# Optimization experiments

Measured on AMD Instinct MI355X. Metric: run time of the kernel, lower is better.

The kernel has to match this reference:

```python
import jax, jax.numpy as jnp
import numpy as np

NUM_HEADS = 12
LN_EPS = 1e-5
SM_EPS = 1e-6


def layer_norm(x, w, b):
    m = x.mean(-1, keepdims=True)
    v = ((x - m) ** 2).mean(-1, keepdims=True)
    return (x - m) / jnp.sqrt(v + LN_EPS) * w + b


def softmax_with_policy(attn, policy):
    # attn: [B,H,N,N], policy: [B,N,1]
    B, H, N, _ = attn.shape
    attn_policy = policy.reshape(B, 1, 1, N)
    eye = jnp.eye(N, dtype=attn.dtype)[None, None]
    attn_policy = attn_policy + (1.0 - attn_policy) * eye
    m = attn.max(axis=-1, keepdims=True)
    e = jnp.exp(attn - m) * attn_policy
    return (e + SM_EPS / N) / (e.sum(axis=-1, keepdims=True) + SM_EPS)


def create_ys(ncdf, n_ref):
    # ncdf: [B, N-1]; returns ys: [B, n_ref-1]
    B = ncdf.shape[0]
    ys = jnp.linspace(0.0, 1.0, n_ref - 1, dtype=ncdf.dtype)[None, :]
    ys_start = jnp.min(ncdf + (ncdf == 0).astype(ncdf.dtype) * 1e8, axis=1, keepdims=True)
    steps = jnp.arange(n_ref - 1, dtype=ncdf.dtype)[None, :]
    return ys_start + (ys * (n_ref - 2) - ys_start * steps) / (n_ref - 2)


def get_unique_indices(indices, max_value):
    # duplicate indices are replaced by max_value, then re-sorted
    B = indices.shape[0]
    s = jnp.sort(indices, axis=1)
    shifted = jnp.concatenate([s[:, 1:], jnp.ones((B, 1), s.dtype)], axis=1)
    uniq = jnp.where(shifted == s, max_value, s)
    return jnp.sort(uniq, axis=1)


def ats_block(x, policy, norm1_w, norm1_b, qkv_w, proj_w, proj_b,
              norm2_w, norm2_b, fc1_w, fc1_b, fc2_w, fc2_b,
              n_tokens, n_ref_tokens):
    B, N, C = x.shape
    H = NUM_HEADS
    dh = C // H
    scale = dh ** -0.5

    xn = layer_norm(x, norm1_w, norm1_b)
    qkv = (xn @ qkv_w).reshape(B, N, 3, H, dh).transpose(2, 0, 3, 1, 4)  # [3,B,H,N,dh]
    qkv = qkv * policy[None, :, None, :, :]
    q, k, v = qkv[0], qkv[1], qkv[2]

    attn = softmax_with_policy(jnp.einsum('bhnd,bhmd->bhnm', q, k) * scale, policy)

    # --- score assignment ---
    v_norm = jnp.linalg.norm(v.transpose(0, 2, 1, 3).reshape(B, N, C), axis=2)  # [B,N]
    sig = attn[:, :, 0, :].sum(axis=1) * v_norm      # CLS attention row summed over heads
    sig = sig[:, 1:]
    sig = sig / sig.sum(axis=1, keepdims=True)
    order = jnp.argsort(sig, axis=1)                 # ascending
    sorted_scores = jnp.take_along_axis(sig, order, axis=1)

    # --- inverse transform sampling ---
    cdf = jnp.cumsum(sorted_scores, axis=1)
    cmin = cdf.min(axis=1, keepdims=True)
    cmax = cdf.max(axis=1, keepdims=True)
    ncdf = (cdf - cmin) / (cmax - cmin)              # [B, N-1]
    ys = create_ys(ncdf, n_ref_tokens)               # [B, n_ref-1]
    diff = (n_ref_tokens - 1) - (N - 1)
    ncdf_p = jnp.pad(ncdf, ((0, 0), (diff, 0))) if diff > 0 else ncdf
    tokens_to_pick = jnp.argmin(jnp.abs(ys[:, :, None] - ncdf_p[:, None, :]), axis=2) - diff

    uniq = get_unique_indices(tokens_to_pick, N - 1)[:, :N - 1]
    ui = uniq[:, :n_tokens - 1]                      # [B, n_tokens-1]

    # reorder attn rows / raw tokens by significance order, pad a zero row at N-1
    oidx = jnp.broadcast_to(order[:, None, :, None], (B, H, N - 1, N))
    attn_sorted = jnp.take_along_axis(attn[:, :, 1:, :], oidx, axis=2)
    attn_tmp = jnp.pad(attn_sorted, ((0, 0), (0, 0), (0, 1), (0, 0)))
    rx_sorted = jnp.take_along_axis(x[:, 1:, :], jnp.broadcast_to(order[:, :, None], (B, N - 1, C)), axis=1)
    rx_tmp = jnp.pad(rx_sorted, ((0, 0), (0, 1), (0, 0)))

    uidx = jnp.broadcast_to(ui[:, None, :, None], (B, H, n_tokens - 1, N))
    attn_sel = jnp.take_along_axis(attn_tmp, uidx, axis=2)
    rx_sel = jnp.take_along_axis(rx_tmp, jnp.broadcast_to(ui[:, :, None], (B, n_tokens - 1, C)), axis=1)

    attn_new = jnp.concatenate([attn[:, :, 0:1, :], attn_sel], axis=2)     # [B,H,n_tokens,N]
    selected_x = jnp.concatenate([x[:, 0:1, :], rx_sel], axis=1)           # [B,n_tokens,C]
    pol_new = (ui != N - 1).astype(x.dtype)[:, :, None]
    pol_new = jnp.pad(pol_new, ((0, 0), (1, 0), (0, 0)), constant_values=1.0)  # [B,n_tokens,1]

    out = jnp.einsum('bhnm,bhmd->bhnd', attn_new, v)
    out = out.transpose(0, 2, 1, 3).reshape(B, n_tokens, C)
    out = (out @ proj_w + proj_b) * pol_new

    x2 = selected_x + out
    h = jax.nn.gelu(layer_norm(x2, norm2_w, norm2_b) @ fc1_w + fc1_b, approximate=False)
    x2 = x2 + (h @ fc2_w + fc2_b) * pol_new
    return x2, pol_new


def setup_inputs() -> dict:
    key = jax.random.key(0)
    ks = jax.random.split(key, 6)
    B, N, C = 8, 785, 768
    init = lambda k, sh, fan: jax.random.normal(k, sh, jnp.float32) * (fan ** -0.5)
    return {
        'x': jax.random.normal(ks[0], (B, N, C), jnp.float32),
        'policy': jnp.ones((B, N, 1), jnp.float32),
        'norm1_w': jnp.ones((C,), jnp.float32),
        'norm1_b': jnp.zeros((C,), jnp.float32),
        'qkv_w': init(ks[1], (C, 3 * C), C),
        'proj_w': init(ks[2], (C, C), C),
        'proj_b': jnp.zeros((C,), jnp.float32),
        'norm2_w': jnp.ones((C,), jnp.float32),
        'norm2_b': jnp.zeros((C,), jnp.float32),
        'fc1_w': init(ks[3], (C, 4 * C), C),
        'fc1_b': jnp.zeros((4 * C,), jnp.float32),
        'fc2_w': init(ks[4], (4 * C, C), 4 * C),
        'fc2_b': jnp.zeros((C,), jnp.float32),
        'n_tokens': 393,
        'n_ref_tokens': 785,
    }


def reference(x, policy, norm1_w, norm1_b, qkv_w, proj_w, proj_b,
              norm2_w, norm2_b, fc1_w, fc1_b, fc2_w, fc2_b,
              n_tokens, n_ref_tokens):
    return ats_block(x, policy, norm1_w, norm1_b, qkv_w, proj_w, proj_b,
                     norm2_w, norm2_b, fc1_w, fc1_b, fc2_w, fc2_b,
                     int(n_tokens), int(n_ref_tokens))
```

## Files before the change

kernel.cpp:

```cpp
#include <hip/hip_runtime.h>
#include <hip/hip_bf16.h>
#include <float.h>
#include <math.h>
#include <stdint.h>

constexpr int B_   = 8;
constexpr int N_   = 785;
constexpr int C_   = 768;
constexpr int H_   = 12;
constexpr int DH_  = 64;
constexpr int NT_  = 393;
constexpr int QKVC = 3 * C_;
constexpr int BN   = B_ * N_;
constexpr int BT   = B_ * NT_;
constexpr int MSEL = N_ - 1;
constexpr float  SCALE_F = 0.125f;
constexpr double LNEPS   = 1e-5;
constexpr double SMEPS   = 1e-6;

#define DEV static __device__ __forceinline__

typedef __hip_bfloat16 bf16;
typedef __attribute__((ext_vector_type(8))) short frag8;
typedef __attribute__((ext_vector_type(4))) float facc4;

DEV double blockReduceSumD(double v, double* scratch, int nw) {
#pragma unroll
  for (int o = 32; o; o >>= 1) v += __shfl_xor(v, o);
  int lane = threadIdx.x & 63, wid = threadIdx.x >> 6;
  __syncthreads();
  if (lane == 0) scratch[wid] = v;
  __syncthreads();
  double r = scratch[0];
  for (int i = 1; i < nw; i++) r += scratch[i];
  return r;
}
DEV double blockReduceMaxD(double v, double* scratch, int nw) {
#pragma unroll
  for (int o = 32; o; o >>= 1) v = fmax(v, __shfl_xor(v, o));
  int lane = threadIdx.x & 63, wid = threadIdx.x >> 6;
  __syncthreads();
  if (lane == 0) scratch[wid] = v;
  __syncthreads();
  double r = scratch[0];
  for (int i = 1; i < nw; i++) r = fmax(r, scratch[i]);
  return r;
}
DEV float blockReduceSumF(float v, float* scratch, int nw) {
#pragma unroll
  for (int o = 32; o; o >>= 1) v += __shfl_xor(v, o);
  int lane = threadIdx.x & 63, wid = threadIdx.x >> 6;
  __syncthreads();
  if (lane == 0) scratch[wid] = v;
  __syncthreads();
  float r = scratch[0];
  for (int i = 1; i < nw; i++) r += scratch[i];
  return r;
}
DEV float blockReduceMaxF(float v, float* scratch, int nw) {
#pragma unroll
  for (int o = 32; o; o >>= 1) v = fmaxf(v, __shfl_xor(v, o));
  int lane = threadIdx.x & 63, wid = threadIdx.x >> 6;
  __syncthreads();
  if (lane == 0) scratch[wid] = v;
  __syncthreads();
  float r = scratch[0];
  for (int i = 1; i < nw; i++) r = fmaxf(r, scratch[i]);
  return r;
}

__global__ __launch_bounds__(256) void ln1_kernel(
    const float* __restrict__ x, const float* __restrict__ w, const float* __restrict__ b,
    double* __restrict__ xn64, bf16* __restrict__ xnb) {
  int row = blockIdx.x;
  int t = threadIdx.x;
  __shared__ double scr[8];
  const float* xr = x + (size_t)row * C_;
  double vals[3];
#pragma unroll
  for (int i = 0; i < 3; i++) vals[i] = (double)xr[t + i * 256];
  double s = vals[0] + vals[1] + vals[2];
  s = blockReduceSumD(s, scr, 4);
  double mean = s / (double)C_;
  double vs = 0.0;
#pragma unroll
  for (int i = 0; i < 3; i++) { double d = vals[i] - mean; vs += d * d; }
  vs = blockReduceSumD(vs, scr, 4);
  double inv = 1.0 / sqrt(vs / (double)C_ + LNEPS);
#pragma unroll
  for (int i = 0; i < 3; i++) {
    int c = t + i * 256;
    double o = (vals[i] - mean) * inv * (double)w[c] + (double)b[c];
    xn64[(size_t)row * C_ + c] = o;
    xnb[(size_t)row * C_ + c] = __float2bfloat16((float)o);
  }
}

__global__ __launch_bounds__(256) void transpose_bf16(
    const float* __restrict__ W, bf16* __restrict__ Wt, int K, int N) {
  __shared__ float tile[32][33];
  int k0 = blockIdx.y * 32, n0 = blockIdx.x * 32;
  int tx = threadIdx.x & 31, ty = threadIdx.x >> 5;
  for (int i = ty; i < 32; i += 8) {
    int k = k0 + i, n = n0 + tx;
    tile[i][tx] = (k < K && n < N) ? W[(size_t)k * N + n] : 0.f;
  }
  __syncthreads();
  for (int i = ty; i < 32; i += 8) {
    int n = n0 + i, k = k0 + tx;
    if (n < N && k < K) Wt[(size_t)n * K + k] = __float2bfloat16(tile[tx][i]);
  }
}

__global__ __launch_bounds__(256) void gemm_bf16(
    const bf16* __restrict__ A, const bf16* __restrict__ Bt,
    float* __restrict__ Cc, const float* __restrict__ bias,
    const float* __restrict__ rowscale, int M, int K, int Ncols) {
  __shared__ short As[64][40];
  __shared__ short Bs[64][40];
  const short* Ap = (const short*)A;
  const short* Bp = (const short*)Bt;
  int t = threadIdx.x;
  int n0 = blockIdx.x * 64;
  int m0 = blockIdx.y * 64;
  int w = t >> 6, l = t & 63;
  int srow = t >> 2;
  int koff = (t & 3) * 8;
  facc4 acc[4] = {{0, 0, 0, 0}, {0, 0, 0, 0}, {0, 0, 0, 0}, {0, 0, 0, 0}};
  int frow = (l & 15);
  int fk = (l >> 4) * 8;
  for (int k0 = 0; k0 < K; k0 += 32) {
    {
      int4 av = make_int4(0, 0, 0, 0);
      if (m0 + srow < M)
        av = *(const int4*)(Ap + (size_t)(m0 + srow) * K + k0 + koff);
      *(int4*)(&As[srow][koff]) = av;
      int4 bv = *(const int4*)(Bp + (size_t)(n0 + srow) * K + k0 + koff);
      *(int4*)(&Bs[srow][koff]) = bv;
    }
    __syncthreads();
    frag8 a = *(frag8*)(&As[w * 16 + frow][fk]);
#pragma unroll
    for (int nt = 0; nt < 4; nt++) {
      frag8 bfr = *(frag8*)(&Bs[nt * 16 + frow][fk]);
      acc[nt] = __builtin_amdgcn_mfma_f32_16x16x32_bf16(a, bfr, acc[nt], 0, 0, 0);
    }
    __syncthreads();
  }
#pragma unroll
  for (int nt = 0; nt < 4; nt++) {
#pragma unroll
    for (int reg = 0; reg < 4; reg++) {
      int row = m0 + w * 16 + (l >> 4) * 4 + reg;
      int col = n0 + nt * 16 + (l & 15);
      if (row < M) {
        float v = acc[nt][reg];
        if (bias) v += bias[col];
        if (rowscale) v *= rowscale[row];
        Cc[(size_t)row * Ncols + col] = v;
      }
    }
  }
}

__global__ __launch_bounds__(256) void q0_kernel(
    const double* __restrict__ xn64, const float* __restrict__ qkvw,
    const float* __restrict__ policy, double* __restrict__ q064) {
  int b = blockIdx.x;
  int jc = blockIdx.y;
  int t = threadIdx.x;
  int jl = t & 63, ks = t >> 6;
  __shared__ double x0[C_];
  __shared__ double part[4][64];
  for (int i = t; i < C_; i += 256) x0[i] = xn64[(size_t)(b * N_) * C_ + i];
  __syncthreads();
  int j = jc * 64 + jl;
  const float* wp = qkvw + j;
  double a = 0.0;
  int c0 = ks * 192;
#pragma unroll 8
  for (int c = c0; c < c0 + 192; c++) a += x0[c] * (double)wp[(size_t)c * QKVC];
  part[ks][jl] = a;
  __syncthreads();
  if (t < 64) {
    double pol = (double)policy[b * N_];
    q064[b * C_ + jc * 64 + t] =
        (part[0][t] + part[1][t] + part[2][t] + part[3][t]) * pol;
  }
}

__global__ __launch_bounds__(256) void g_kernel(
    const double* __restrict__ q064, const float* __restrict__ qkvw,
    double* __restrict__ g64) {
  int bh = blockIdx.x;
  int b = bh / H_, h = bh % H_;
  int t = threadIdx.x;
  __shared__ double qh[DH_];
  if (t < DH_) qh[t] = q064[b * C_ + h * DH_ + t];
  __syncthreads();
  for (int c = t; c < C_; c += 256) {
    const float* wp = qkvw + (size_t)c * QKVC + C_ + h * DH_;
    double a = 0.0;
#pragma unroll 8
    for (int d = 0; d < DH_; d++) a += qh[d] * (double)wp[d];
    g64[(size_t)bh * C_ + c] = a;
  }
}

__global__ __launch_bounds__(256) void logits_kernel(
    const double* __restrict__ xn64, const double* __restrict__ g64,
    const float* __restrict__ policy, double* __restrict__ l64) {
  int row = blockIdx.x;
  int b = row / N_;
  int n = row % N_;
  int t = threadIdx.x;
  int w = t >> 6, lane = t & 63;
  __shared__ double xr[C_];
  for (int i = t; i < C_; i += 256) xr[i] = xn64[(size_t)row * C_ + i];
  __syncthreads();
  double pol = (double)policy[row];
#pragma unroll
  for (int hh = 0; hh < 3; hh++) {
    int h = w + hh * 4;
    const double* gp = g64 + (size_t)(b * H_ + h) * C_;
    double p = 0.0;
#pragma unroll 4
    for (int i = lane; i < C_; i += 64) p += xr[i] * gp[i];
#pragma unroll
    for (int o = 32; o; o >>= 1) p += __shfl_xor(p, o);
    if (lane == 0) l64[(size_t)(b * H_ + h) * N_ + n] = 0.125 * pol * p;
  }
}

__global__ __launch_bounds__(256) void vnorm_kernel(
    const double* __restrict__ xn64, const float* __restrict__ qkvw,
    const float* __restrict__ policy, double* __restrict__ vnorm2) {
  __shared__ double scr[8];
  int r0 = blockIdx.x * 8;
  int t = threadIdx.x;
  double acc[8][3] = {};
  const double* xb = xn64 + (size_t)r0 * C_;
  for (int c = 0; c < C_; c += 2) {
    const float* wp0 = qkvw + (size_t)c * QKVC + 2 * C_;
    const float* wp1 = wp0 + QKVC;
    double w00 = (double)wp0[t], w01 = (double)wp0[t + 256], w02 = (double)wp0[t + 512];
    double w10 = (double)wp1[t], w11 = (double)wp1[t + 256], w12 = (double)wp1[t + 512];
#pragma unroll
    for (int r = 0; r < 8; r++) {
      double x0 = xb[(size_t)r * C_ + c];
      double x1 = xb[(size_t)r * C_ + c + 1];
      acc[r][0] += x0 * w00; acc[r][1] += x0 * w01; acc[r][2] += x0 * w02;
      acc[r][0] += x1 * w10; acc[r][1] += x1 * w11; acc[r][2] += x1 * w12;
    }
  }
#pragma unroll
  for (int r = 0; r < 8; r++) {
    double p = acc[r][0] * acc[r][0] + acc[r][1] * acc[r][1] + acc[r][2] * acc[r][2];
    double s = blockReduceSumD(p, scr, 4);
    if (t == 0) {
      double pol = (double)policy[r0 + r];
      vnorm2[r0 + r] = s * pol * pol;
    }
  }
}

__global__ __launch_bounds__(256) void softmax0_kernel(
    double* __restrict__ l64, const float* __restrict__ policy) {
  int bh = blockIdx.x;
  int b = bh / H_;
  double* lp = l64 + (size_t)bh * N_;
  __shared__ double scr[8];
  int t = threadIdx.x;
  double mx = -1e300;
  for (int n = t; n < N_; n += 256) mx = fmax(mx, lp[n]);
  mx = blockReduceMaxD(mx, scr, 4);
  double ssum = 0.0;
  for (int n = t; n < N_; n += 256) {
    double pol = (double)policy[b * N_ + n];
    double w = (n == 0) ? 1.0 : pol;
    double e = exp(lp[n] - mx) * w;
    lp[n] = e;
    ssum += e;
  }
  ssum = blockReduceSumD(ssum, scr, 4);
  double denom = ssum + SMEPS;
  double addc = SMEPS / (double)N_;
  for (int n = t; n < N_; n += 256) lp[n] = (lp[n] + addc) / denom;
}

__global__ __launch_bounds__(1024) void select_kernel(
    const double* __restrict__ p0, const double* __restrict__ vnorm2,
    int* __restrict__ selidx, float* __restrict__ poln, float* __restrict__ out_pol) {
  int b = blockIdx.x;
  int t = threadIdx.x;
  __shared__ double sigv[MSEL];
  __shared__ double svals[MSEL];
  __shared__ double nc[MSEL];
  __shared__ int    ord[MSEL];
  __shared__ int    pick[MSEL];
  __shared__ int    spick[MSEL];
  __shared__ int    uq[MSEL];
  __shared__ int    suq[MSEL];
  __shared__ double sh_ys;

  if (t < MSEL) {
    int n = t + 1;
    double s = 0.0;
#pragma unroll
    for (int h = 0; h < H_; h++) s += p0[(size_t)(b * H_ + h) * N_ + n];
    sigv[t] = s * sqrt(vnorm2[b * N_ + n]);
  }
  __syncthreads();
  if (t < MSEL) {
    double v = sigv[t];
    int rank = 0;
    for (int i = 0; i < MSEL; i++) {
      double vi = sigv[i];
      rank += (vi < v) || (vi == v && i < t);
    }
    ord[rank] = t;
    svals[rank] = v;
  }
  __syncthreads();
  if (t == 0) {
    double a = 0.0;
    for (int i = 0; i < MSEL; i++) { a += svals[i]; svals[i] = a; }
  }
  __syncthreads();
  {
    double c0 = svals[0], cN = svals[MSEL - 1];
    if (t < MSEL) nc[t] = (svals[t] - c0) / (cN - c0);
  }
  __syncthreads();
  if (t == 0) {
    double m = 1e300;
    for (int i = 0; i < MSEL; i++) {
      double v = nc[i];
      if (v == 0.0) v += 100000000.0;
      m = fmin(m, v);
    }
    sh_ys = m;
  }
  __syncthreads();
  if (t < MSEL) {
    double s = sh_ys;
    double ysj = (t == MSEL - 1) ? 1.0 : (double)t / 783.0;
    double y = s + (ysj * 783.0 - s * (double)t) / 783.0;
    double bd = 1e300;
    int bi = 0;
    for (int i = 0; i < MSEL; i++) {
      double d = fabs(y - nc[i]);
      if (d < bd) { bd = d; bi = i; }
    }
    pick[t] = bi;
  }
  __syncthreads();
  if (t < MSEL) {
    int p = pick[t];
    int rank = 0;
    for (int i = 0; i < MSEL; i++) {
      int pi = pick[i];
      rank += (pi < p) || (pi == p && i < t);
    }
    spick[rank] = p;
  }
  __syncthreads();
  if (t < MSEL) {
    int s = spick[t];
    int nxt = (t < MSEL - 1) ? spick[t + 1] : 1;
    uq[t] = (nxt == s) ? MSEL : s;
  }
  __syncthreads();
  if (t < MSEL) {
    int u = uq[t];
    int rank = 0;
    for (int i = 0; i < MSEL; i++) {
      int ui = uq[i];
      rank += (ui < u) || (ui == u && i < t);
    }
    suq[rank] = u;
  }
  __syncthreads();
  if (t < NT_) {
    int sel, polI;
    if (t == 0) { sel = 0; polI = 1; }
    else {
      int ut = suq[t - 1];
      polI = (ut != MSEL) ? 1 : 0;
      sel = polI ? (ord[ut] + 1) : -1;
    }
    selidx[b * NT_ + t] = sel;
    poln[b * NT_ + t] = (float)polI;
    out_pol[b * NT_ + t] = (float)polI;
  }
}

__global__ __launch_bounds__(256) void flash_kernel(
    const float* __restrict__ qkv, const int* __restrict__ selidx,
    const float* __restrict__ policy, bf16* __restrict__ attn_bf) {
  int bh = blockIdx.y;
  int b = bh / H_, h = bh % H_;
  int j0 = blockIdx.x * 64;
  int t = threadIdx.x;
  __shared__ float Qs[64][68];
  __shared__ float KVs[64][68];
  __shared__ float Ps[64][68];
  __shared__ float Vsum[64];
  int lm = t >> 2;
  int kb = (t & 3) * 16;
  {
    int j = j0 + lm;
    int r = (j < NT_) ? selidx[b * NT_ + j] : -1;
    if (r < 0) r = 0;
    const float* qp = qkv + (size_t)(b * N_ + r) * QKVC + h * DH_ + kb;
    float4 v0 = *(const float4*)(qp + 0);
    float4 v1 = *(const float4*)(qp + 4);
    float4 v2 = *(const float4*)(qp + 8);
    float4 v3 = *(const float4*)(qp + 12);
    Qs[kb + 0][lm] = v0.x; Qs[kb + 1][lm] = v0.y; Qs[kb + 2][lm] = v0.z; Qs[kb + 3][lm] = v0.w;
    Qs[kb + 4][lm] = v1.x; Qs[kb + 5][lm] = v1.y; Qs[kb + 6][lm] = v1.z; Qs[kb + 7][lm] = v1.w;
    Qs[kb + 8][lm] = v2.x; Qs[kb + 9][lm] = v2.y; Qs[kb +10][lm] = v2.z; Qs[kb +11][lm] = v2.w;
    Qs[kb +12][lm] = v3.x; Qs[kb +13][lm] = v3.y; Qs[kb +14][lm] = v3.z; Qs[kb +15][lm] = v3.w;
  }
  if (t < 64) Vsum[t] = 0.f;
  int tm = (t >> 4) << 2, tn = (t & 15) << 2;
  int rrow[4];
#pragma unroll
  for (int i = 0; i < 4; i++) {
    int j = j0 + tm + i;
    rrow[i] = (j < NT_) ? selidx[b * NT_ + j] : -1;
  }
  float m_run[4] = {-1e30f, -1e30f, -1e30f, -1e30f};
  float s_run[4] = {0.f, 0.f, 0.f, 0.f};
  float O[4][4] = {{0.f}};
  for (int n0 = 0; n0 < 832; n0 += 64) {
    __syncthreads();
    {
      int n = n0 + lm;
      bool ok = n < N_;
      const float* kp = qkv + (size_t)(b * N_ + (ok ? n : 0)) * QKVC + C_ + h * DH_ + kb;
      float4 v0 = ok ? *(const float4*)(kp + 0)  : make_float4(0, 0, 0, 0);
      float4 v1 = ok ? *(const float4*)(kp + 4)  : make_float4(0, 0, 0, 0);
      float4 v2 = ok ? *(const float4*)(kp + 8)  : make_float4(0, 0, 0, 0);
      float4 v3 = ok ? *(const float4*)(kp + 12) : make_float4(0, 0, 0, 0);
      KVs[kb + 0][lm] = v0.x; KVs[kb + 1][lm] = v0.y; KVs[kb + 2][lm] = v0.z; KVs[kb + 3][lm] = v0.w;
      KVs[kb + 4][lm] = v1.x; KVs[kb + 5][lm] = v1.y; KVs[kb + 6][lm] = v1.z; KVs[kb + 7][lm] = v1.w;
      KVs[kb + 8][lm] = v2.x; KVs[kb + 9][lm] = v2.y; KVs[kb +10][lm] = v2.z; KVs[kb +11][lm] = v2.w;
      KVs[kb +12][lm] = v3.x; KVs[kb +13][lm] = v3.y; KVs[kb +14][lm] = v3.z; KVs[kb +15][lm] = v3.w;
    }
    __syncthreads();
    float S[4][4] = {{0.f}};
#pragma unroll 16
    for (int k = 0; k < 64; k++) {
      float a0 = Qs[k][tm + 0], a1 = Qs[k][tm + 1], a2 = Qs[k][tm + 2], a3 = Qs[k][tm + 3];
      float b0 = KVs[k][tn + 0], b1 = KVs[k][tn + 1], b2 = KVs[k][tn + 2], b3 = KVs[k][tn + 3];
      S[0][0] += a0 * b0; S[0][1] += a0 * b1; S[0][2] += a0 * b2; S[0][3] += a0 * b3;
      S[1][0] += a1 * b0; S[1][1] += a1 * b1; S[1][2] += a1 * b2; S[1][3] += a1 * b3;
      S[2][0] += a2 * b0; S[2][1] += a2 * b1; S[2][2] += a2 * b2; S[2][3] += a2 * b3;
      S[3][0] += a3 * b0; S[3][1] += a3 * b1; S[3][2] += a3 * b2; S[3][3] += a3 * b3;
    }
    float tmax[4];
#pragma unroll
    for (int i = 0; i < 4; i++) {
      float mx = -1e30f;
#pragma unroll
      for (int jj = 0; jj < 4; jj++) {
        int n = n0 + tn + jj;
        float v = (n < N_) ? S[i][jj] * SCALE_F : -1e30f;
        S[i][jj] = v;
        mx = fmaxf(mx, v);
      }
      tmax[i] = mx;
    }
#pragma unroll
    for (int o = 1; o < 16; o <<= 1) {
#pragma unroll
      for (int i = 0; i < 4; i++) tmax[i] = fmaxf(tmax[i], __shfl_xor(tmax[i], o));
    }
    float m_new[4], scl[4], psum[4];
#pragma unroll
    for (int i = 0; i < 4; i++) {
      m_new[i] = fmaxf(m_run[i], tmax[i]);
      scl[i] = expf(m_run[i] - m_new[i]);
      psum[i] = 0.f;
    }
    float polv[4];
#pragma unroll
    for (int jj = 0; jj < 4; jj++) {
      int n = n0 + tn + jj;
      polv[jj] = (n < N_) ? policy[b * N_ + n] : 0.f;
    }
#pragma unroll
    for (int i = 0; i < 4; i++) {
#pragma unroll
      for (int jj = 0; jj < 4; jj++) {
        int n = n0 + tn + jj;
        float w = (n == rrow[i]) ? 1.f : polv[jj];
        float e = expf(S[i][jj] - m_new[i]) * w;
        S[i][jj] = e;
        psum[i] += e;
      }
    }
#pragma unroll
    for (int o = 1; o < 16; o <<= 1) {
#pragma unroll
      for (int i = 0; i < 4; i++) psum[i] += __shfl_xor(psum[i], o);
    }
#pragma unroll
    for (int i = 0; i < 4; i++) {
      s_run[i] = s_run[i] * scl[i] + psum[i];
      m_run[i] = m_new[i];
    }
    __syncthreads();
#pragma unroll
    for (int i = 0; i < 4; i++) {
#pragma unroll
      for (int jj = 0; jj < 4; jj++) Ps[tn + jj][tm + i] = S[i][jj];
    }
    {
      int n = n0 + lm;
      bool ok = n < N_;
      const float* vp = qkv + (size_t)(b * N_ + (ok ? n : 0)) * QKVC + 2 * C_ + h * DH_ + kb;
      float4 v0 = ok ? *(const float4*)(vp + 0)  : make_float4(0, 0, 0, 0);
      float4 v1 = ok ? *(const float4*)(vp + 4)  : make_float4(0, 0, 0, 0);
      float4 v2 = ok ? *(const float4*)(vp + 8)  : make_float4(0, 0, 0, 0);
      float4 v3 = ok ? *(const float4*)(vp + 12) : make_float4(0, 0, 0, 0);
      *(float4*)(&KVs[lm][kb + 0])  = v0;
      *(float4*)(&KVs[lm][kb + 4])  = v1;
      *(float4*)(&KVs[lm][kb + 8])  = v2;
      *(float4*)(&KVs[lm][kb + 12]) = v3;
    }
    __syncthreads();
    if (t < 64) {
      float a = 0.f;
#pragma unroll 16
      for (int k = 0; k < 64; k++) a += KVs[k][t];
      Vsum[t] += a;
    }
#pragma unroll
    for (int i = 0; i < 4; i++) {
#pragma unroll
      for (int jj = 0; jj < 4; jj++) O[i][jj] *= scl[i];
    }
#pragma unroll 16
    for (int k = 0; k < 64; k++) {
      float a0 = Ps[k][tm + 0], a1 = Ps[k][tm + 1], a2 = Ps[k][tm + 2], a3 = Ps[k][tm + 3];
      float b0 = KVs[k][tn + 0], b1 = KVs[k][tn + 1], b2 = KVs[k][tn + 2], b3 = KVs[k][tn + 3];
      O[0][0] += a0 * b0; O[0][1] += a0 * b1; O[0][2] += a0 * b2; O[0][3] += a0 * b3;
      O[1][0] += a1 * b0; O[1][1] += a1 * b1; O[1][2] += a1 * b2; O[1][3] += a1 * b3;
      O[2][0] += a2 * b0; O[2][1] += a2 * b1; O[2][2] += a2 * b2; O[2][3] += a2 * b3;
      O[3][0] += a3 * b0; O[3][1] += a3 * b1; O[3][2] += a3 * b2; O[3][3] += a3 * b3;
    }
  }
  __syncthreads();
  float addc = 1e-6f / (float)N_;
#pragma unroll
  for (int i = 0; i < 4; i++) {
    int j = j0 + tm + i;
    if (j >= NT_) continue;
    float denom = s_run[i] + 1e-6f;
#pragma unroll
    for (int jj = 0; jj < 4; jj++) {
      float val = (O[i][jj] + addc * Vsum[tn + jj]) / denom;
      attn_bf[(size_t)(b * NT_ + j) * C_ + h * DH_ + tn + jj] = __float2bfloat16(val);
    }
  }
}

__global__ __launch_bounds__(256) void e2_kernel(
    const float* __restrict__ cbuf, const float* __restrict__ poln,
    const int* __restrict__ selidx, const float* __restrict__ x, float* __restrict__ x2) {
  int row = blockIdx.x;
  int t = threadIdx.x;
  int b = row / NT_;
  int r = selidx[row];
  float pn = poln[row];
  for (int i = t; i < C_; i += 256) {
    float sx = (r >= 0) ? x[(size_t)(b * N_ + r) * C_ + i] : 0.f;
    x2[(size_t)row * C_ + i] = sx + cbuf[(size_t)row * C_ + i] * pn;
  }
}

__global__ __launch_bounds__(256) void ln2_kernel(
    const float* __restrict__ xin, const float* __restrict__ w, const float* __restrict__ b,
    bf16* __restrict__ xoutb) {
  int row = blockIdx.x;
  int t = threadIdx.x;
  __shared__ float scr[8];
  const float* xr = xin + (size_t)row * C_;
  float vals[3];
#pragma unroll
  for (int i = 0; i < 3; i++) vals[i] = xr[t + i * 256];
  float s = vals[0] + vals[1] + vals[2];
  s = blockReduceSumF(s, scr, 4);
  float mean = s / (float)C_;
  float vs = 0.f;
#pragma unroll
  for (int i = 0; i < 3; i++) { float d = vals[i] - mean; vs += d * d; }
  vs = blockReduceSumF(vs, scr, 4);
  float sd = sqrtf(vs / (float)C_ + 1e-5f);
#pragma unroll
  for (int i = 0; i < 3; i++) {
    int c = t + i * 256;
    xoutb[(size_t)row * C_ + c] =
        __float2bfloat16((vals[i] - mean) / sd * w[c] + b[c]);
  }
}

DEV float gelu_exact(float v) { return 0.5f * v * (1.0f + erff(v * 0.70710678118654752f)); }

__global__ __launch_bounds__(256) void gelu_kernel(
    const float* __restrict__ h, bf16* __restrict__ hb) {
  size_t i = (size_t)blockIdx.x * 256 + threadIdx.x;
  float4 v = ((const float4*)h)[i];
  ushort4 o;
  o.x = __hip_bfloat16_raw(__float2bfloat16(gelu_exact(v.x))).x;
  o.y = __hip_bfloat16_raw(__float2bfloat16(gelu_exact(v.y))).x;
  o.z = __hip_bfloat16_raw(__float2bfloat16(gelu_exact(v.z))).x;
  o.w = __hip_bfloat16_raw(__float2bfloat16(gelu_exact(v.w))).x;
  ((ushort4*)hb)[i] = o;
}

__global__ __launch_bounds__(256) void e4_kernel(
    const float* __restrict__ x2, const float* __restrict__ cbuf,
    const float* __restrict__ poln, float* __restrict__ out) {
  int row = blockIdx.x;
  int t = threadIdx.x;
  float pn = poln[row];
  for (int i = t; i < C_; i += 256) {
    float v = x2[(size_t)row * C_ + i] + cbuf[(size_t)row * C_ + i] * pn;
    out[(size_t)row * C_ + i] = v;
  }
}

extern "C" void kernel_launch(void* const* d_in, const int* in_sizes, int n_in,
                              void* d_out, int out_size, void* d_ws, size_t ws_size,
                              hipStream_t stream) {
  const float* x      = (const float*)d_in[0];
  const float* policy = (const float*)d_in[1];
  const float* n1w    = (const float*)d_in[2];
  const float* n1b    = (const float*)d_in[3];
  const float* qkvw   = (const float*)d_in[4];
  const float* projw  = (const float*)d_in[5];
  const float* projb  = (const float*)d_in[6];
  const float* n2w    = (const float*)d_in[7];
  const float* n2b    = (const float*)d_in[8];
  const float* fc1w   = (const float*)d_in[9];
  const float* fc1b   = (const float*)d_in[10];
  const float* fc2w   = (const float*)d_in[11];
  const float* fc2b   = (const float*)d_in[12];

  char* ws = (char*)d_ws;
  size_t off = 0;
  auto alloc = [&](size_t bytes) {
    size_t o = off;
    off += (bytes + 255) & ~(size_t)255;
    return o;
  };

  double* xn64    = (double*)(ws + alloc((size_t)BN * C_ * 8));
  bf16*   xnb     = (bf16*)(ws + alloc((size_t)BN * C_ * 2));
  float*  qkv32   = (float*)(ws + alloc((size_t)BN * QKVC * 4));
  double* vnorm2  = (double*)(ws + alloc((size_t)BN * 8));
  double* q064    = (double*)(ws + alloc((size_t)B_ * C_ * 8));
  double* g64     = (double*)(ws + alloc((size_t)B_ * H_ * C_ * 8));
  double* l64     = (double*)(ws + alloc((size_t)B_ * H_ * N_ * 8));
  int*    selidx  = (int*)(ws + alloc((size_t)BT * 4));
  float*  poln    = (float*)(ws + alloc((size_t)BT * 4));
  bf16*   attn_bf = (bf16*)(ws + alloc((size_t)BT * C_ * 2));
  float*  cbuf    = (float*)(ws + alloc((size_t)BT * C_ * 4));
  float*  x2      = (float*)(ws + alloc((size_t)BT * C_ * 4));
  bf16*   qkvw_t  = (bf16*)(ws + alloc((size_t)QKVC * C_ * 2));
  bf16*   projw_t = (bf16*)(ws + alloc((size_t)C_ * C_ * 2));
  bf16*   fc1w_t  = (bf16*)(ws + alloc((size_t)4 * C_ * C_ * 2));
  bf16*   fc2w_t  = (bf16*)(ws + alloc((size_t)C_ * 4 * C_ * 2));
  bf16*   xn2b    = (bf16*)(ws + alloc((size_t)BT * C_ * 2));
  float*  h32     = (float*)(ws + alloc((size_t)BT * 4 * C_ * 4));
  bf16*   h_bf    = (bf16*)(ws + alloc((size_t)BT * 4 * C_ * 2));
  if (off > ws_size) return;

  float* out_x = (float*)d_out;
  float* out_p = out_x + (size_t)BT * C_;

  transpose_bf16<<<dim3(QKVC / 32, C_ / 32), 256, 0, stream>>>(qkvw, qkvw_t, C_, QKVC);
  transpose_bf16<<<dim3(C_ / 32, C_ / 32), 256, 0, stream>>>(projw, projw_t, C_, C_);
  transpose_bf16<<<dim3(4 * C_ / 32, C_ / 32), 256, 0, stream>>>(fc1w, fc1w_t, C_, 4 * C_);
  transpose_bf16<<<dim3(C_ / 32, 4 * C_ / 32), 256, 0, stream>>>(fc2w, fc2w_t, 4 * C_, C_);

  ln1_kernel<<<BN, 256, 0, stream>>>(x, n1w, n1b, xn64, xnb);

  {
    dim3 g(QKVC / 64, (BN + 63) / 64);
    gemm_bf16<<<g, 256, 0, stream>>>(xnb, qkvw_t, qkv32, nullptr, policy, BN, C_, QKVC);
  }

  q0_kernel<<<dim3(B_, C_ / 64), 256, 0, stream>>>(xn64, qkvw, policy, q064);
  g_kernel<<<B_ * H_, 256, 0, stream>>>(q064, qkvw, g64);
  logits_kernel<<<BN, 256, 0, stream>>>(xn64, g64, policy, l64);
  vnorm_kernel<<<BN / 8, 256, 0, stream>>>(xn64, qkvw, policy, vnorm2);
  softmax0_kernel<<<B_ * H_, 256, 0, stream>>>(l64, policy);
  select_kernel<<<B_, 1024, 0, stream>>>(l64, vnorm2, selidx, poln, out_p);

  {
    dim3 g((NT_ + 63) / 64, B_ * H_);
    flash_kernel<<<g, 256, 0, stream>>>(qkv32, selidx, policy, attn_bf);
  }

  {
    dim3 g(C_ / 64, (BT + 63) / 64);
    gemm_bf16<<<g, 256, 0, stream>>>(attn_bf, projw_t, cbuf, projb, nullptr, BT, C_, C_);
  }
  e2_kernel<<<BT, 256, 0, stream>>>(cbuf, poln, selidx, x, x2);
  ln2_kernel<<<BT, 256, 0, stream>>>(x2, n2w, n2b, xn2b);
  {
    dim3 g(4 * C_ / 64, (BT + 63) / 64);
    gemm_bf16<<<g, 256, 0, stream>>>(xn2b, fc1w_t, h32, fc1b, nullptr, BT, C_, 4 * C_);
  }
  gelu_kernel<<<(BT * 4 * C_) / 1024, 256, 0, stream>>>(h32, h_bf);
  {
    dim3 g(C_ / 64, (BT + 63) / 64);
    gemm_bf16<<<g, 256, 0, stream>>>(h_bf, fc2w_t, cbuf, fc2b, nullptr, BT, 4 * C_, C_);
  }
  e4_kernel<<<BT, 256, 0, stream>>>(x2, cbuf, poln, out_x);
}
```

Measured before the change: 990.7 us.

## Use bf16 MFMA for QK^T and PV in the flash attention kernel

Rewrites the flash attention inner loops to convert Q, K, V and the probability tile to bf16 in shared memory and compute both matmuls with 16x16x32 bf16 MFMA instructions instead of scalar fp32 FMAs. The row-wise online softmax is remapped onto the MFMA accumulator layout. The aim is to move the dominant attention FLOPs onto matrix cores and halve the shared-memory footprint. In exchange, the attention scores and probabilities are computed at bf16 precision. The global loads also become scalar per-element reads with conversion rather than float4 vectors.

```diff
diff --git a/kernel.cpp b/kernel.cpp
--- a/kernel.cpp
+++ b/kernel.cpp
@@ -23,6 +23,13 @@
 typedef __hip_bfloat16 bf16;
 typedef __attribute__((ext_vector_type(8))) short frag8;
 typedef __attribute__((ext_vector_type(4))) float facc4;
+
+DEV short f2b(float v) { return (short)__hip_bfloat16_raw(__float2bfloat16(v)).x; }
+DEV float b2f(short s) {
+  union { unsigned int u; float f; } cv;
+  cv.u = ((unsigned int)(unsigned short)s) << 16;
+  return cv.f;
+}
 
 DEV double blockReduceSumD(double v, double* scratch, int nw) {
 #pragma unroll
@@ -402,167 +409,160 @@
   int b = bh / H_, h = bh % H_;
   int j0 = blockIdx.x * 64;
   int t = threadIdx.x;
-  __shared__ float Qs[64][68];
-  __shared__ float KVs[64][68];
-  __shared__ float Ps[64][68];
+  int w = t >> 6, l = t & 63;
+  __shared__ short Qs[64][72];
+  __shared__ short Ks[64][72];
+  __shared__ short Ps[64][72];
+  __shared__ short Vs[64][72];
+  __shared__ float pol_s[64];
   __shared__ float Vsum[64];
-  int lm = t >> 2;
-  int kb = (t & 3) * 16;
+
   {
-    int j = j0 + lm;
+    int jr = t >> 2, d0 = (t & 3) * 16;
+    int j = j0 + jr;
     int r = (j < NT_) ? selidx[b * NT_ + j] : -1;
     if (r < 0) r = 0;
-    const float* qp = qkv + (size_t)(b * N_ + r) * QKVC + h * DH_ + kb;
-    float4 v0 = *(const float4*)(qp + 0);
-    float4 v1 = *(const float4*)(qp + 4);
-    float4 v2 = *(const float4*)(qp + 8);
-    float4 v3 = *(const float4*)(qp + 12);
-    Qs[kb + 0][lm] = v0.x; Qs[kb + 1][lm] = v0.y; Qs[kb + 2][lm] = v0.z; Qs[kb + 3][lm] = v0.w;
-    Qs[kb + 4][lm] = v1.x; Qs[kb + 5][lm] = v1.y; Qs[kb + 6][lm] = v1.z; Qs[kb + 7][lm] = v1.w;
-    Qs[kb + 8][lm] = v2.x; Qs[kb + 9][lm] = v2.y; Qs[kb +10][lm] = v2.z; Qs[kb +11][lm] = v2.w;
-    Qs[kb +12][lm] = v3.x; Qs[kb +13][lm] = v3.y; Qs[kb +14][lm] = v3.z; Qs[kb +15][lm] = v3.w;
+    const float* qp = qkv + (size_t)(b * N_ + r) * QKVC + h * DH_ + d0;
+#pragma unroll
+    for (int i = 0; i < 16; i++) Qs[jr][d0 + i] = f2b(qp[i]);
   }
   if (t < 64) Vsum[t] = 0.f;
-  int tm = (t >> 4) << 2, tn = (t & 15) << 2;
+
+  int frow = l & 15, fk = (l >> 4) * 8;
+  int base_r = w * 16 + (l >> 4) * 4;
+  int coln = l & 15;
+
   int rrow[4];
 #pragma unroll
-  for (int i = 0; i < 4; i++) {
-    int j = j0 + tm + i;
-    rrow[i] = (j < NT_) ? selidx[b * NT_ + j] : -1;
+  for (int r = 0; r < 4; r++) {
+    int j = j0 + base_r + r;
+    rrow[r] = (j < NT_) ? selidx[b * NT_ + j] : -1;
   }
   float m_run[4] = {-1e30f, -1e30f, -1e30f, -1e30f};
   float s_run[4] = {0.f, 0.f, 0.f, 0.f};
-  float O[4][4] = {{0.f}};
+  facc4 Oacc[4] = {{0, 0, 0, 0}, {0, 0, 0, 0}, {0, 0, 0, 0}, {0, 0, 0, 0}};
+
   for (int n0 = 0; n0 < 832; n0 += 64) {
+    {
+      int nr = t >> 2, d0 = (t & 3) * 16;
+      int n = n0 + nr;
+      bool ok = n < N_;
+      const float* kp = qkv + (size_t)(b * N_ + (ok ? n : 0)) * QKVC + C_ + h * DH_ + d0;
+#pragma unroll
+      for (int i = 0; i < 16; i++) Ks[nr][d0 + i] = f2b(ok ? kp[i] : 0.f);
+    }
+    if (t < 64) {
+      int n = n0 + t;
+      pol_s[t] = (n < N_) ? policy[b * N_ + n] : 0.f;
+    }
     __syncthreads();
+
+    facc4 Sacc[4] = {{0, 0, 0, 0}, {0, 0, 0, 0}, {0, 0, 0, 0}, {0, 0, 0, 0}};
+#pragma unroll
+    for (int k0 = 0; k0 < 64; k0 += 32) {
+      frag8 a = *(frag8*)(&Qs[w * 16 + frow][k0 + fk]);
+#pragma unroll
+      for (int nt = 0; nt < 4; nt++) {
+        frag8 bb = *(frag8*)(&Ks[nt * 16 + frow][k0 + fk]);
+        Sacc[nt] = __builtin_amdgcn_mfma_f32_16x16x32_bf16(a, bb, Sacc[nt], 0, 0, 0);
+      }
+    }
+    float S[4][4];
+    float tmax[4] = {-1e30f, -1e30f, -1e30f, -1e30f};
+#pragma unroll
+    for (int nt = 0; nt < 4; nt++) {
+#pragma unroll
+      for (int r = 0; r < 4; r++) {
+        int n = n0 + nt * 16 + coln;
+        float v = (n < N_) ? Sacc[nt][r] * SCALE_F : -1e30f;
+        S[nt][r] = v;
+        tmax[r] = fmaxf(tmax[r], v);
+      }
+    }
+#pragma unroll
+    for (int o = 1; o < 16; o <<= 1) {
+#pragma unroll
+      for (int r = 0; r < 4; r++) tmax[r] = fmaxf(tmax[r], __shfl_xor(tmax[r], o));
+    }
+    float m_new[4], scl[4], psum[4];
+#pragma unroll
+    for (int r = 0; r < 4; r++) {
+      m_new[r] = fmaxf(m_run[r], tmax[r]);
+      scl[r] = expf(m_run[r] - m_new[r]);
+      psum[r] = 0.f;
+    }
+#pragma unroll
+    for (int nt = 0; nt < 4; nt++) {
+      float pol = pol_s[nt * 16 + coln];
+      int n = n0 + nt * 16 + coln;
+#pragma unroll
+      for (int r = 0; r < 4; r++) {
+        float wgt = (n == rrow[r]) ? 1.f : pol;
+        float e = expf(S[nt][r] - m_new[r]) * wgt;
+        S[nt][r] = e;
+        psum[r] += e;
+      }
+    }
+#pragma unroll
+    for (int o = 1; o < 16; o <<= 1) {
+#pragma unroll
+      for (int r = 0; r < 4; r++) psum[r] += __shfl_xor(psum[r], o);
+    }
+#pragma unroll
+    for (int r = 0; r < 4; r++) {
+      s_run[r] = s_run[r] * scl[r] + psum[r];
+      m_run[r] = m_new[r];
+    }
+    __syncthreads();
+
+#pragma unroll
+    for (int nt = 0; nt < 4; nt++) {
+#pragma unroll
+      for (int r = 0; r < 4; r++) Ps[base_r + r][nt * 16 + coln] = f2b(S[nt][r]);
+    }
     {
-      int n = n0 + lm;
+      int nr = t >> 2, d0 = (t & 3) * 16;
+      int n = n0 + nr;
       bool ok = n < N_;
-      const float* kp = qkv + (size_t)(b * N_ + (ok ? n : 0)) * QKVC + C_ + h * DH_ + kb;
-      float4 v0 = ok ? *(const float4*)(kp + 0)  : make_float4(0, 0, 0, 0);
-      float4 v1 = ok ? *(const float4*)(kp + 4)  : make_float4(0, 0, 0, 0);
-      float4 v2 = ok ? *(const float4*)(kp + 8)  : make_float4(0, 0, 0, 0);
-      float4 v3 = ok ? *(const float4*)(kp + 12) : make_float4(0, 0, 0, 0);
-      KVs[kb + 0][lm] = v0.x; KVs[kb + 1][lm] = v0.y; KVs[kb + 2][lm] = v0.z; KVs[kb + 3][lm] = v0.w;
-      KVs[kb + 4][lm] = v1.x; KVs[kb + 5][lm] = v1.y; KVs[kb + 6][lm] = v1.z; KVs[kb + 7][lm] = v1.w;
-      KVs[kb + 8][lm] = v2.x; KVs[kb + 9][lm] = v2.y; KVs[kb +10][lm] = v2.z; KVs[kb +11][lm] = v2.w;
-      KVs[kb +12][lm] = v3.x; KVs[kb +13][lm] = v3.y; KVs[kb +14][lm] = v3.z; KVs[kb +15][lm] = v3.w;
+      const float* vp = qkv + (size_t)(b * N_ + (ok ? n : 0)) * QKVC + 2 * C_ + h * DH_ + d0;
+#pragma unroll
+      for (int i = 0; i < 16; i++) Vs[d0 + i][nr] = f2b(ok ? vp[i] : 0.f);
     }
     __syncthreads();
-    float S[4][4] = {{0.f}};
-#pragma unroll 16
-    for (int k = 0; k < 64; k++) {
-      float a0 = Qs[k][tm + 0], a1 = Qs[k][tm + 1], a2 = Qs[k][tm + 2], a3 = Qs[k][tm + 3];
-      float b0 = KVs[k][tn + 0], b1 = KVs[k][tn + 1], b2 = KVs[k][tn + 2], b3 = KVs[k][tn + 3];
-      S[0][0] += a0 * b0; S[0][1] += a0 * b1; S[0][2] += a0 * b2; S[0][3] += a0 * b3;
-      S[1][0] += a1 * b0; S[1][1] += a1 * b1; S[1][2] += a1 * b2; S[1][3] += a1 * b3;
-      S[2][0] += a2 * b0; S[2][1] += a2 * b1; S[2][2] += a2 * b2; S[2][3] += a2 * b3;
-      S[3][0] += a3 * b0; S[3][1] += a3 * b1; S[3][2] += a3 * b2; S[3][3] += a3 * b3;
-    }
-    float tmax[4];
-#pragma unroll
-    for (int i = 0; i < 4; i++) {
-      float mx = -1e30f;
-#pragma unroll
-      for (int jj = 0; jj < 4; jj++) {
-        int n = n0 + tn + jj;
-        float v = (n < N_) ? S[i][jj] * SCALE_F : -1e30f;
-        S[i][jj] = v;
-        mx = fmaxf(mx, v);
-      }
-      tmax[i] = mx;
-    }
-#pragma unroll
-    for (int o = 1; o < 16; o <<= 1) {
-#pragma unroll
-      for (int i = 0; i < 4; i++) tmax[i] = fmaxf(tmax[i], __shfl_xor(tmax[i], o));
-    }
-    float m_new[4], scl[4], psum[4];
-#pragma unroll
-    for (int i = 0; i < 4; i++) {
-      m_new[i] = fmaxf(m_run[i], tmax[i]);
-      scl[i] = expf(m_run[i] - m_new[i]);
-      psum[i] = 0.f;
-    }
-    float polv[4];
-#pragma unroll
-    for (int jj = 0; jj < 4; jj++) {
-      int n = n0 + tn + jj;
-      polv[jj] = (n < N_) ? policy[b * N_ + n] : 0.f;
-    }
-#pragma unroll
-    for (int i = 0; i < 4; i++) {
-#pragma unroll
-      for (int jj = 0; jj < 4; jj++) {
-        int n = n0 + tn + jj;
-        float w = (n == rrow[i]) ? 1.f : polv[jj];
-        float e = expf(S[i][jj] - m_new[i]) * w;
-        S[i][jj] = e;
-        psum[i] += e;
-      }
-    }
-#pragma unroll
-    for (int o = 1; o < 16; o <<= 1) {
-#pragma unroll
-      for (int i = 0; i < 4; i++) psum[i] += __shfl_xor(psum[i], o);
-    }
-#pragma unroll
-    for (int i = 0; i < 4; i++) {
-      s_run[i] = s_run[i] * scl[i] + psum[i];
-      m_run[i] = m_new[i];
-    }
-    __syncthreads();
-#pragma unroll
-    for (int i = 0; i < 4; i++) {
-#pragma unroll
-      for (int jj = 0; jj < 4; jj++) Ps[tn + jj][tm + i] = S[i][jj];
-    }
-    {
-      int n = n0 + lm;
-      bool ok = n < N_;
-      const float* vp = qkv + (size_t)(b * N_ + (ok ? n : 0)) * QKVC + 2 * C_ + h * DH_ + kb;
-      float4 v0 = ok ? *(const float4*)(vp + 0)  : make_float4(0, 0, 0, 0);
-      float4 v1 = ok ? *(const float4*)(vp + 4)  : make_float4(0, 0, 0, 0);
-      float4 v2 = ok ? *(const float4*)(vp + 8)  : make_float4(0, 0, 0, 0);
-      float4 v3 = ok ? *(const float4*)(vp + 12) : make_float4(0, 0, 0, 0);
-      *(float4*)(&KVs[lm][kb + 0])  = v0;
-      *(float4*)(&KVs[lm][kb + 4])  = v1;
-      *(float4*)(&KVs[lm][kb + 8])  = v2;
-      *(float4*)(&KVs[lm][kb + 12]) = v3;
-    }
-    __syncthreads();
+
     if (t < 64) {
       float a = 0.f;
 #pragma unroll 16
-      for (int k = 0; k < 64; k++) a += KVs[k][t];
+      for (int k = 0; k < 64; k++) a += b2f(Vs[t][k]);
       Vsum[t] += a;
     }
 #pragma unroll
-    for (int i = 0; i < 4; i++) {
-#pragma unroll
-      for (int jj = 0; jj < 4; jj++) O[i][jj] *= scl[i];
-    }
-#pragma unroll 16
-    for (int k = 0; k < 64; k++) {
-      float a0 = Ps[k][tm + 0], a1 = Ps[k][tm + 1], a2 = Ps[k][tm + 2], a3 = Ps[k][tm + 3];
-      float b0 = KVs[k][tn + 0], b1 = KVs[k][tn + 1], b2 = KVs[k][tn + 2], b3 = KVs[k][tn + 3];
-      O[0][0] += a0 * b0; O[0][1] += a0 * b1; O[0][2] += a0 * b2; O[0][3] += a0 * b3;
-      O[1][0] += a1 * b0; O[1][1] += a1 * b1; O[1][2] += a1 * b2; O[1][3] += a1 * b3;
-      O[2][0] += a2 * b0; O[2][1] += a2 * b1; O[2][2] += a2 * b2; O[2][3] += a2 * b3;
-      O[3][0] += a3 * b0; O[3][1] += a3 * b1; O[3][2] += a3 * b2; O[3][3] += a3 * b3;
+    for (int dt = 0; dt < 4; dt++) {
+#pragma unroll
+      for (int r = 0; r < 4; r++) Oacc[dt][r] *= scl[r];
+    }
+#pragma unroll
+    for (int k0 = 0; k0 < 64; k0 += 32) {
+      frag8 a = *(frag8*)(&Ps[w * 16 + frow][k0 + fk]);
+#pragma unroll
+      for (int dt = 0; dt < 4; dt++) {
+        frag8 bb = *(frag8*)(&Vs[dt * 16 + frow][k0 + fk]);
+        Oacc[dt] = __builtin_amdgcn_mfma_f32_16x16x32_bf16(a, bb, Oacc[dt], 0, 0, 0);
+      }
     }
   }
   __syncthreads();
   float addc = 1e-6f / (float)N_;
 #pragma unroll
-  for (int i = 0; i < 4; i++) {
-    int j = j0 + tm + i;
+  for (int r = 0; r < 4; r++) {
+    int j = j0 + base_r + r;
     if (j >= NT_) continue;
-    float denom = s_run[i] + 1e-6f;
-#pragma unroll
-    for (int jj = 0; jj < 4; jj++) {
-      float val = (O[i][jj] + addc * Vsum[tn + jj]) / denom;
-      attn_bf[(size_t)(b * NT_ + j) * C_ + h * DH_ + tn + jj] = __float2bfloat16(val);
+    float denom = s_run[r] + 1e-6f;
+#pragma unroll
+    for (int dt = 0; dt < 4; dt++) {
+      int d = dt * 16 + coln;
+      float val = (Oacc[dt][r] + addc * Vsum[d]) / denom;
+      attn_bf[(size_t)(b * NT_ + j) * C_ + h * DH_ + d] = __float2bfloat16(val);
     }
   }
 }
```

Result: faster. 892.6 us (-9.9%).
